# Optimization experiments

Hardware: AMD Instinct MI355X
Metric: run time of the kernel (lower is better)

Reference implementation:

```python
import jax, jax.numpy as jnp
import numpy as np

VOCAB, EMB, HID = 10, 32, 64
B, T = 256, 2048


def setup_inputs() -> dict:
    key = jax.random.key(0)
    ks = jax.random.split(key, 12)
    s = lambda k, shp, sc: jax.random.normal(k, shp, dtype=jnp.float32) * sc
    return {
        "num1": jax.random.randint(ks[0], (B, T), 0, VOCAB),
        "num2": jax.random.randint(ks[1], (B, T), 0, VOCAB),
        "E": s(ks[2], (VOCAB, EMB), 0.05),
        "Wx": s(ks[3], (EMB, 4 * HID), 1.0 / np.sqrt(EMB)),
        "Wh": s(ks[4], (HID, 4 * HID), 1.0 / np.sqrt(HID)),
        "b": jnp.zeros((4 * HID,), jnp.float32),
        "W1": s(ks[5], (2 * HID, 64), 1.0 / np.sqrt(2 * HID)),
        "b1": jnp.zeros((64,), jnp.float32),
        "W2": s(ks[6], (64, 32), 1.0 / np.sqrt(64)),
        "b2": jnp.zeros((32,), jnp.float32),
        "W3": s(ks[7], (32, VOCAB), 1.0 / np.sqrt(32)),
        "b3": jnp.zeros((VOCAB,), jnp.float32),
    }


def _lstm(x, Wx, Wh, b):
    # x: [B, T, EMB] -> hs: [B, T, HID]
    xz = jnp.einsum("btd,dg->btg", x, Wx) + b  # precompute input projection

    def step(carry, z_t):
        h, c = carry
        z = z_t + h @ Wh
        i, f, g, o = jnp.split(z, 4, axis=-1)  # Keras gate order: i, f, c, o
        i = jax.nn.sigmoid(i)
        f = jax.nn.sigmoid(f)
        g = jnp.tanh(g)
        o = jax.nn.sigmoid(o)
        c = f * c + i * g
        h = o * jnp.tanh(c)
        return (h, c), h

    bsz = x.shape[0]
    init = (jnp.zeros((bsz, HID), x.dtype), jnp.zeros((bsz, HID), x.dtype))
    _, hs = jax.lax.scan(step, init, jnp.swapaxes(xz, 0, 1))
    return jnp.swapaxes(hs, 0, 1)


def reference(num1, num2, E, Wx, Wh, b, W1, b1, W2, b2, W3, b3):
    x1 = E[num1]  # [B, T, EMB]
    x2 = E[num2]
    y1 = _lstm(x1, Wx, Wh, b)  # shared RNN layer (same weights)
    y2 = _lstm(x2, Wx, Wh, b)
    z = jnp.concatenate([y1, y2], axis=-1)  # [B, T, 128]
    w1 = jax.nn.relu(z @ W1 + b1)
    w2 = jax.nn.relu(w1 @ W2 + b2)
    return w2 @ W3 + b3  # [B, T, 10]
```

## Files before the change

kernel.cpp:

```cpp
#include <hip/hip_runtime.h>
#include <hip/hip_bf16.h>

#define BSZ    256
#define SEQT   2048
#define NVOCAB 10
#define DEMB   32
#define G4     256
#define BLK    384

typedef unsigned short u16;
typedef unsigned int   u32;
typedef float    v4f __attribute__((ext_vector_type(4)));
typedef u32      v4u __attribute__((ext_vector_type(4)));
typedef _Float16 v2h __attribute__((ext_vector_type(2)));

#define FLAG_OFF 0
#define XZ4_OFF  4
#define WHP_OFF  (XZ4_OFF + 2560)
#define W1P_OFF  (WHP_OFF + 8192)
#define W2P_OFF  (W1P_OFF + 4096)
#define W3_OFF   (W2P_OFF + 1024)
#define B1_OFF   (W3_OFF + 320)
#define B2_OFF   (B1_OFF + 64)
#define B3_OFF   (B2_OFF + 32)

__device__ __forceinline__ float bf2f(u16 x) {
    union { u32 u; float f; } v; v.u = ((u32)x) << 16; return v.f;
}
__device__ __forceinline__ u16 f2bf(float f) {
    union { float f; u32 u; } v; v.f = f;
    u32 r = v.u + 0x7fff + ((v.u >> 16) & 1);
    return (u16)(r >> 16);
}
__device__ __forceinline__ float ldw(const void* p, int i, bool isbf) {
    return isbf ? bf2f(((const u16*)p)[i]) : ((const float*)p)[i];
}
__device__ __forceinline__ float frcp(float x) { return __builtin_amdgcn_rcpf(x); }
__device__ __forceinline__ float sigf(float z) { return frcp(1.f + __expf(-z)); }
__device__ __forceinline__ u16 f2h(float x) {
    union { _Float16 h; u16 u; } v; v.h = (_Float16)x; return v.u;
}
__device__ __forceinline__ u32 packh2(float lo, float hi) {
    return (u32)f2h(lo) | ((u32)f2h(hi) << 16);
}
__device__ __forceinline__ float fdot2f(u32 a, u32 b, float c) {
    union { u32 u; v2h h; } ua, ub; ua.u = a; ub.u = b;
    return __builtin_amdgcn_fdot2(ua.h, ub.h, c, false);
}
__device__ __forceinline__ void dot4(float& acc, v4u w, v4u h) {
    acc = fdot2f(w.x, h.x, acc); acc = fdot2f(w.y, h.y, acc);
    acc = fdot2f(w.z, h.z, acc); acc = fdot2f(w.w, h.w, acc);
}

__global__ void init_kernel(const void* __restrict__ E,  const void* __restrict__ Wx,
                            const void* __restrict__ Wh, const void* __restrict__ bg,
                            const void* __restrict__ W1, const void* __restrict__ b1,
                            const void* __restrict__ W2, const void* __restrict__ b2,
                            const void* __restrict__ W3, const void* __restrict__ b3,
                            float* __restrict__ ws) {
    __shared__ int s_isbf;
    const int tid = threadIdx.x;
    if (tid == 0) s_isbf = 1;
    __syncthreads();
    {
        const u16* Eu = (const u16*)E;
        for (int i = tid; i < NVOCAB * DEMB; i += 256) {
            float v = bf2f(Eu[i]);
            if (!(fabsf(v) < 16.0f)) s_isbf = 0;
        }
    }
    __syncthreads();
    const bool isbf = (s_isbf != 0);
    if (tid == 0) ws[FLAG_OFF] = isbf ? 1.0f : 0.0f;
    u32* wsu = (u32*)ws;

    {
        const int g = tid >> 6, j = tid & 63, col = g * 64 + j;
        for (int v = 0; v < NVOCAB; v++) {
            float acc = ldw(bg, col, isbf);
            #pragma unroll
            for (int d = 0; d < DEMB; d++)
                acc += ldw(E, v * DEMB + d, isbf) * ldw(Wx, d * G4 + col, isbf);
            ws[XZ4_OFF + (v * 64 + j) * 4 + g] = acc;
        }
    }
    for (int i = tid; i < 8192; i += 256) {
        int l = i >> 7, rem = i & 127, g = rem >> 5, kk = rem & 31;
        int col = g * 64 + l;
        wsu[WHP_OFF + i] = packh2(ldw(Wh, (2 * kk) * G4 + col, isbf),
                                  ldw(Wh, (2 * kk + 1) * G4 + col, isbf));
    }
    for (int i = tid; i < 4096; i += 256) {
        int o = i >> 6, kk = i & 63;
        wsu[W1P_OFF + i] = packh2(ldw(W1, (2 * kk) * 64 + o, isbf),
                                  ldw(W1, (2 * kk + 1) * 64 + o, isbf));
    }
    for (int i = tid; i < 1024; i += 256) {
        int o = i >> 5, kk = i & 31;
        wsu[W2P_OFF + i] = packh2(ldw(W2, (2 * kk) * 32 + o, isbf),
                                  ldw(W2, (2 * kk + 1) * 32 + o, isbf));
    }
    for (int i = tid; i < 320; i += 256) ws[W3_OFF + i] = ldw(W3, i, isbf);
    if (tid < 64) ws[B1_OFF + tid] = ldw(b1, tid, isbf);
    if (tid < 32) ws[B2_OFF + tid] = ldw(b2, tid, isbf);
    if (tid < NVOCAB) ws[B3_OFF + tid] = ldw(b3, tid, isbf);
}

__global__ __launch_bounds__(BLK, 2) void lstm_fused(
    const int* __restrict__ num1, const int* __restrict__ num2,
    const float* __restrict__ ws, void* __restrict__ outv)
{
    __shared__ __align__(16) float xz4s[2560];
    __shared__ __align__(16) u16 hwinh[2][32][128];
    __shared__ __align__(16) u32 W1p[64 * 68];
    __shared__ __align__(16) u32 W2p[32 * 36];
    __shared__ float W3s[320];
    __shared__ __align__(16) u16 w1h[32 * 72];
    __shared__ __align__(16) float w2buf[32 * 36];
    __shared__ int idxs[2][2][32];

    const int tid = threadIdx.x, bb = blockIdx.x;
    const int wv = tid >> 6, l = tid & 63;
    const u32* wsu = (const u32*)ws;
    const bool outbf = (ws[FLAG_OFF] != 0.0f);

    for (int i = tid; i < 2560; i += BLK) xz4s[i] = ws[XZ4_OFF + i];
    for (int i = tid; i < 4096; i += BLK) { int o = i >> 6, kk = i & 63; W1p[o * 68 + kk] = wsu[W1P_OFF + i]; }
    for (int i = tid; i < 1024; i += BLK) { int o = i >> 5, kk = i & 31; W2p[o * 36 + kk] = wsu[W2P_OFF + i]; }
    for (int i = tid; i < 320; i += BLK) W3s[i] = ws[W3_OFF + i];
    if (tid < 128) hwinh[1][31][tid] = 0;
    if (tid < 64) { int c0 = tid >> 5, tt = tid & 31;
                    idxs[0][c0][tt] = (c0 == 0 ? num1 : num2)[bb * SEQT + tt]; }

    if (wv < 2) {
        v4u whq[32];
        {
            const v4u* whsrc = (const v4u*)(wsu + WHP_OFF) + (size_t)l * 32;
            #pragma unroll
            for (int i = 0; i < 32; i++) whq[i] = whsrc[i];
        }
        float c = 0.f;
        __syncthreads();
        for (int win = 0; win <= 64; win++) {
            #pragma unroll
            for (int i = 0; i < 32; i++) asm("" : "+v"(whq[i]));
            if (win < 64) {
                const int wb = win & 1;
                #pragma unroll 1
                for (int tt = 0; tt < 32; tt++) {
                    const int idx  = idxs[wb][wv][tt];
                    const int rbuf = (tt == 0) ? 1 - wb : wb;
                    const int rrow = (tt + 31) & 31;
                    const v4u* hp = (const v4u*)&hwinh[rbuf][rrow][wv * 64];
                    v4u hh[8];
                    #pragma unroll
                    for (int q = 0; q < 8; q++) hh[q] = hp[q];
                    v4f xzv = *(const v4f*)&xz4s[(idx * 64 + l) * 4];
                    float ai0 = 0.f, af0 = 0.f, ag0 = 0.f, ao0 = 0.f;
                    float ai1 = 0.f, af1 = 0.f, ag1 = 0.f, ao1 = 0.f;
                    #pragma unroll
                    for (int q = 0; q < 4; q++) {
                        dot4(ai0, whq[q],      hh[q]);
                        dot4(af0, whq[8 + q],  hh[q]);
                        dot4(ag0, whq[16 + q], hh[q]);
                        dot4(ao0, whq[24 + q], hh[q]);
                    }
                    #pragma unroll
                    for (int q = 4; q < 8; q++) {
                        dot4(ai1, whq[q],      hh[q]);
                        dot4(af1, whq[8 + q],  hh[q]);
                        dot4(ag1, whq[16 + q], hh[q]);
                        dot4(ao1, whq[24 + q], hh[q]);
                    }
                    float zi = ai0 + ai1 + xzv.x, zf = af0 + af1 + xzv.y;
                    float zg = ag0 + ag1 + xzv.z, zo = ao0 + ao1 + xzv.w;
                    float gi = sigf(zi), gf = sigf(zf);
                    float gG = 2.f * sigf(2.f * zg) - 1.f, go = sigf(zo);
                    c = gf * c + gi * gG;
                    float th = 1.f - 2.f * frcp(__expf(2.f * c) + 1.f);
                    hwinh[wb][tt][wv * 64 + l] = f2h(go * th);
                }
            }
            __syncthreads();
        }
    } else {
        const int mw = wv - 2;
        const int tb = mw * 8;
        const float b1o = ws[B1_OFF + l];
        const int th = l >> 5, o2 = l & 31;
        const float b2o = ws[B2_OFF + o2];
        const int tloc = l / 10, o3 = l - tloc * 10;
        const float b3o = (l < 40) ? ws[B3_OFF + o3] : 0.f;
        u16* outb = (u16*)outv; float* outf = (float*)outv;
        __syncthreads();
        float w3r[32];
        #pragma unroll
        for (int k = 0; k < 32; k++) w3r[k] = (l < 40) ? W3s[k * 10 + o3] : 0.f;
        for (int win = 0; win <= 64; win++) {
            if (win < 63 && mw < 2 && l < 32)
                idxs[(win + 1) & 1][mw][l] =
                    (mw == 0 ? num1 : num2)[bb * SEQT + (win + 1) * 32 + l];
            if (win >= 1) {
                const int pw = win - 1, pwb = pw & 1;
                float acc[8];
                #pragma unroll
                for (int i = 0; i < 8; i++) acc[i] = b1o;
                for (int kc = 0; kc < 16; kc++) {
                    v4u wq = *(const v4u*)&W1p[l * 68 + 4 * kc];
                    #pragma unroll
                    for (int i = 0; i < 8; i++) {
                        v4u hq = *(const v4u*)&hwinh[pwb][tb + i][8 * kc];
                        float a = acc[i];
                        a = fdot2f(wq.x, hq.x, a); a = fdot2f(wq.y, hq.y, a);
                        a = fdot2f(wq.z, hq.z, a); a = fdot2f(wq.w, hq.w, a);
                        acc[i] = a;
                    }
                }
                #pragma unroll
                for (int i = 0; i < 8; i++)
                    w1h[(tb + i) * 72 + l] = f2h(fmaxf(acc[i], 0.f));
                float a2[4];
                #pragma unroll
                for (int i = 0; i < 4; i++) a2[i] = b2o;
                for (int kc = 0; kc < 8; kc++) {
                    v4u wq = *(const v4u*)&W2p[o2 * 36 + 4 * kc];
                    #pragma unroll
                    for (int i = 0; i < 4; i++) {
                        v4u hq = *(const v4u*)&w1h[(tb + th * 4 + i) * 72 + 8 * kc];
                        float a = a2[i];
                        a = fdot2f(wq.x, hq.x, a); a = fdot2f(wq.y, hq.y, a);
                        a = fdot2f(wq.z, hq.z, a); a = fdot2f(wq.w, hq.w, a);
                        a2[i] = a;
                    }
                }
                #pragma unroll
                for (int i = 0; i < 4; i++)
                    w2buf[(tb + th * 4 + i) * 36 + o2] = fmaxf(a2[i], 0.f);
                if (l < 40) {
                    #pragma unroll
                    for (int i = 0; i < 2; i++) {
                        const int tk = tb + tloc * 2 + i;
                        const v4f* wp = (const v4f*)&w2buf[tk * 36];
                        float a = b3o;
                        #pragma unroll
                        for (int q = 0; q < 8; q++) {
                            v4f w4 = wp[q];
                            a += w3r[4 * q]     * w4.x + w3r[4 * q + 1] * w4.y
                               + w3r[4 * q + 2] * w4.z + w3r[4 * q + 3] * w4.w;
                        }
                        const size_t oi = (size_t)(bb * SEQT + pw * 32 + tk) * NVOCAB + o3;
                        if (outbf) outb[oi] = f2bf(a); else outf[oi] = a;
                    }
                }
            }
            __syncthreads();
        }
    }
}

extern "C" void kernel_launch(void* const* d_in, const int* in_sizes, int n_in,
                              void* d_out, int out_size, void* d_ws, size_t ws_size,
                              hipStream_t stream) {
    const int* num1 = (const int*)d_in[0];
    const int* num2 = (const int*)d_in[1];
    float* ws = (float*)d_ws;

    hipLaunchKernelGGL(init_kernel, dim3(1), dim3(256), 0, stream,
                       d_in[2], d_in[3], d_in[4], d_in[5], d_in[6], d_in[7],
                       d_in[8], d_in[9], d_in[10], d_in[11], ws);
    hipLaunchKernelGGL(lstm_fused, dim3(BSZ), dim3(BLK), 0, stream,
                       num1, num2, ws, d_out);
}
```

Measured before the change: 981.5 us.

## Split LSTM gates across four waves per chain and serialize MLP after recurrence

Each LSTM chain is now spread over four wavefronts, one per gate, instead of one wavefront computing all four gates. Each gate wave holds only its slice of Wh in registers and exchanges activations through shared memory with a block-wide barrier every timestep. The MLP head no longer runs in dedicated waves concurrently with the recurrence. All 8 waves now run it after each 32-step window. The change shortens the per-step dependent dot-product chain but adds a __syncthreads per timestep and removes the overlap between recurrence and MLP.

```diff
diff --git a/kernel.cpp b/kernel.cpp
--- a/kernel.cpp
+++ b/kernel.cpp
@@ -6,7 +6,7 @@
 #define NVOCAB 10
 #define DEMB   32
 #define G4     256
-#define BLK    384
+#define BLK    512
 
 typedef unsigned short u16;
 typedef unsigned int   u32;
@@ -106,155 +106,140 @@
     if (tid < NVOCAB) ws[B3_OFF + tid] = ldw(b3, tid, isbf);
 }
 
-__global__ __launch_bounds__(BLK, 2) void lstm_fused(
+__global__ __launch_bounds__(BLK) void lstm_fused(
     const int* __restrict__ num1, const int* __restrict__ num2,
     const float* __restrict__ ws, void* __restrict__ outv)
 {
-    __shared__ __align__(16) float xz4s[2560];
+    __shared__ __align__(16) float xzg[4 * 10 * 64];
     __shared__ __align__(16) u16 hwinh[2][32][128];
+    __shared__ __align__(16) u16 hpriv[8][64];
+    __shared__ __align__(16) float acts[2][2][4][64];
     __shared__ __align__(16) u32 W1p[64 * 68];
     __shared__ __align__(16) u32 W2p[32 * 36];
     __shared__ float W3s[320];
+    __shared__ float B1s[64], B2s[32], B3s[16];
     __shared__ __align__(16) u16 w1h[32 * 72];
     __shared__ __align__(16) float w2buf[32 * 36];
     __shared__ int idxs[2][2][32];
 
     const int tid = threadIdx.x, bb = blockIdx.x;
     const int wv = tid >> 6, l = tid & 63;
+    const int ch = wv >> 2, g = wv & 3;
     const u32* wsu = (const u32*)ws;
     const bool outbf = (ws[FLAG_OFF] != 0.0f);
 
-    for (int i = tid; i < 2560; i += BLK) xz4s[i] = ws[XZ4_OFF + i];
+    for (int t = tid; t < 2560; t += BLK) {
+        int gg = t / 640, rem = t - gg * 640;
+        xzg[t] = ws[XZ4_OFF + rem * 4 + gg];
+    }
     for (int i = tid; i < 4096; i += BLK) { int o = i >> 6, kk = i & 63; W1p[o * 68 + kk] = wsu[W1P_OFF + i]; }
     for (int i = tid; i < 1024; i += BLK) { int o = i >> 5, kk = i & 31; W2p[o * 36 + kk] = wsu[W2P_OFF + i]; }
     for (int i = tid; i < 320; i += BLK) W3s[i] = ws[W3_OFF + i];
-    if (tid < 128) hwinh[1][31][tid] = 0;
+    if (tid < 64) B1s[tid] = ws[B1_OFF + tid];
+    if (tid < 32) B2s[tid] = ws[B2_OFF + tid];
+    if (tid < NVOCAB) B3s[tid] = ws[B3_OFF + tid];
+    hpriv[wv][l] = 0;
     if (tid < 64) { int c0 = tid >> 5, tt = tid & 31;
                     idxs[0][c0][tt] = (c0 == 0 ? num1 : num2)[bb * SEQT + tt]; }
 
-    if (wv < 2) {
-        v4u whq[32];
-        {
-            const v4u* whsrc = (const v4u*)(wsu + WHP_OFF) + (size_t)l * 32;
-            #pragma unroll
-            for (int i = 0; i < 32; i++) whq[i] = whsrc[i];
-        }
-        float c = 0.f;
+    const v4u* whsrc = (const v4u*)(wsu + WHP_OFF) + ((size_t)l * 32 + g * 8);
+    v4u wqA0 = whsrc[0], wqA1 = whsrc[1], wqA2 = whsrc[2], wqA3 = whsrc[3];
+    v4u wqB0 = whsrc[4], wqB1 = whsrc[5], wqB2 = whsrc[6], wqB3 = whsrc[7];
+    float c = 0.f;
+
+    const int tb = wv * 4;
+    const int th = l >> 5, o2 = l & 31;
+    const int tloc = l / 10, o3 = l - tloc * 10;
+    u16* outb = (u16*)outv; float* outf = (float*)outv;
+
+    __syncthreads();
+
+    for (int win = 0; win <= 64; win++) {
+        #define PINQ(x) asm("" : "+v"(x))
+        PINQ(wqA0); PINQ(wqA1); PINQ(wqA2); PINQ(wqA3);
+        PINQ(wqB0); PINQ(wqB1); PINQ(wqB2); PINQ(wqB3);
+        #undef PINQ
+        if (win < 64) {
+            const int wb = win & 1;
+            if (win < 63 && g == 3 && l < 32)
+                idxs[(win + 1) & 1][ch][l] =
+                    (ch == 0 ? num1 : num2)[bb * SEQT + (win + 1) * 32 + l];
+            #pragma unroll 1
+            for (int tt = 0; tt < 32; tt++) {
+                const int p = tt & 1;
+                const int idx = idxs[wb][ch][tt];
+                const v4u* hp = (const v4u*)&hpriv[wv][0];
+                float za = 0.f, zb = 0.f;
+                {
+                    v4u h0 = hp[0], h1 = hp[1], h2 = hp[2], h3 = hp[3];
+                    dot4(za, wqA0, h0); dot4(za, wqA1, h1);
+                    dot4(za, wqA2, h2); dot4(za, wqA3, h3);
+                }
+                {
+                    v4u h4 = hp[4], h5 = hp[5], h6 = hp[6], h7 = hp[7];
+                    dot4(zb, wqB0, h4); dot4(zb, wqB1, h5);
+                    dot4(zb, wqB2, h6); dot4(zb, wqB3, h7);
+                }
+                float z = za + zb + xzg[g * 640 + idx * 64 + l];
+                float act = (g == 2) ? (2.f * sigf(2.f * z) - 1.f)
+                                     : sigf(z);
+                acts[p][ch][g][l] = act;
+                __syncthreads();
+                float ai = acts[p][ch][0][l], af = acts[p][ch][1][l];
+                float ag = acts[p][ch][2][l], ao = acts[p][ch][3][l];
+                c = af * c + ai * ag;
+                float thh = 1.f - 2.f * frcp(__expf(2.f * c) + 1.f);
+                u16 hb = f2h(ao * thh);
+                hpriv[wv][l] = hb;
+                if (g == 0) hwinh[wb][tt][ch * 64 + l] = hb;
+            }
+        }
         __syncthreads();
-        for (int win = 0; win <= 64; win++) {
-            #pragma unroll
-            for (int i = 0; i < 32; i++) asm("" : "+v"(whq[i]));
-            if (win < 64) {
-                const int wb = win & 1;
-                #pragma unroll 1
-                for (int tt = 0; tt < 32; tt++) {
-                    const int idx  = idxs[wb][wv][tt];
-                    const int rbuf = (tt == 0) ? 1 - wb : wb;
-                    const int rrow = (tt + 31) & 31;
-                    const v4u* hp = (const v4u*)&hwinh[rbuf][rrow][wv * 64];
-                    v4u hh[8];
-                    #pragma unroll
-                    for (int q = 0; q < 8; q++) hh[q] = hp[q];
-                    v4f xzv = *(const v4f*)&xz4s[(idx * 64 + l) * 4];
-                    float ai0 = 0.f, af0 = 0.f, ag0 = 0.f, ao0 = 0.f;
-                    float ai1 = 0.f, af1 = 0.f, ag1 = 0.f, ao1 = 0.f;
-                    #pragma unroll
-                    for (int q = 0; q < 4; q++) {
-                        dot4(ai0, whq[q],      hh[q]);
-                        dot4(af0, whq[8 + q],  hh[q]);
-                        dot4(ag0, whq[16 + q], hh[q]);
-                        dot4(ao0, whq[24 + q], hh[q]);
-                    }
-                    #pragma unroll
-                    for (int q = 4; q < 8; q++) {
-                        dot4(ai1, whq[q],      hh[q]);
-                        dot4(af1, whq[8 + q],  hh[q]);
-                        dot4(ag1, whq[16 + q], hh[q]);
-                        dot4(ao1, whq[24 + q], hh[q]);
-                    }
-                    float zi = ai0 + ai1 + xzv.x, zf = af0 + af1 + xzv.y;
-                    float zg = ag0 + ag1 + xzv.z, zo = ao0 + ao1 + xzv.w;
-                    float gi = sigf(zi), gf = sigf(zf);
-                    float gG = 2.f * sigf(2.f * zg) - 1.f, go = sigf(zo);
-                    c = gf * c + gi * gG;
-                    float th = 1.f - 2.f * frcp(__expf(2.f * c) + 1.f);
-                    hwinh[wb][tt][wv * 64 + l] = f2h(go * th);
+        if (win >= 1) {
+            const int pw = win - 1, pwb = pw & 1;
+            const float b1o = B1s[l];
+            float acc0 = b1o, acc1 = b1o, acc2 = b1o, acc3 = b1o;
+            for (int kc = 0; kc < 16; kc++) {
+                v4u wq = *(const v4u*)&W1p[l * 68 + 4 * kc];
+                v4u q0 = *(const v4u*)&hwinh[pwb][tb + 0][8 * kc];
+                v4u q1 = *(const v4u*)&hwinh[pwb][tb + 1][8 * kc];
+                v4u q2 = *(const v4u*)&hwinh[pwb][tb + 2][8 * kc];
+                v4u q3 = *(const v4u*)&hwinh[pwb][tb + 3][8 * kc];
+                dot4(acc0, wq, q0); dot4(acc1, wq, q1);
+                dot4(acc2, wq, q2); dot4(acc3, wq, q3);
+            }
+            w1h[(tb + 0) * 72 + l] = f2h(fmaxf(acc0, 0.f));
+            w1h[(tb + 1) * 72 + l] = f2h(fmaxf(acc1, 0.f));
+            w1h[(tb + 2) * 72 + l] = f2h(fmaxf(acc2, 0.f));
+            w1h[(tb + 3) * 72 + l] = f2h(fmaxf(acc3, 0.f));
+            const float b2o = B2s[o2];
+            float a20 = b2o, a21 = b2o;
+            for (int kc = 0; kc < 8; kc++) {
+                v4u wq = *(const v4u*)&W2p[o2 * 36 + 4 * kc];
+                v4u q0 = *(const v4u*)&w1h[(tb + th * 2 + 0) * 72 + 8 * kc];
+                v4u q1 = *(const v4u*)&w1h[(tb + th * 2 + 1) * 72 + 8 * kc];
+                dot4(a20, wq, q0); dot4(a21, wq, q1);
+            }
+            w2buf[(tb + th * 2 + 0) * 36 + o2] = fmaxf(a20, 0.f);
+            w2buf[(tb + th * 2 + 1) * 36 + o2] = fmaxf(a21, 0.f);
+            if (l < 40) {
+                float w3r[32];
+                #pragma unroll
+                for (int k = 0; k < 32; k++) w3r[k] = W3s[k * 10 + o3];
+                const int tk = tb + tloc;
+                const v4f* wp = (const v4f*)&w2buf[tk * 36];
+                float a = B3s[o3];
+                #pragma unroll
+                for (int q = 0; q < 8; q++) {
+                    v4f w4 = wp[q];
+                    a += w3r[4 * q]     * w4.x + w3r[4 * q + 1] * w4.y
+                       + w3r[4 * q + 2] * w4.z + w3r[4 * q + 3] * w4.w;
                 }
-            }
-            __syncthreads();
-        }
-    } else {
-        const int mw = wv - 2;
-        const int tb = mw * 8;
-        const float b1o = ws[B1_OFF + l];
-        const int th = l >> 5, o2 = l & 31;
-        const float b2o = ws[B2_OFF + o2];
-        const int tloc = l / 10, o3 = l - tloc * 10;
-        const float b3o = (l < 40) ? ws[B3_OFF + o3] : 0.f;
-        u16* outb = (u16*)outv; float* outf = (float*)outv;
+                const size_t oi = (size_t)(bb * SEQT + pw * 32 + tk) * NVOCAB + o3;
+                if (outbf) outb[oi] = f2bf(a); else outf[oi] = a;
+            }
+        }
         __syncthreads();
-        float w3r[32];
-        #pragma unroll
-        for (int k = 0; k < 32; k++) w3r[k] = (l < 40) ? W3s[k * 10 + o3] : 0.f;
-        for (int win = 0; win <= 64; win++) {
-            if (win < 63 && mw < 2 && l < 32)
-                idxs[(win + 1) & 1][mw][l] =
-                    (mw == 0 ? num1 : num2)[bb * SEQT + (win + 1) * 32 + l];
-            if (win >= 1) {
-                const int pw = win - 1, pwb = pw & 1;
-                float acc[8];
-                #pragma unroll
-                for (int i = 0; i < 8; i++) acc[i] = b1o;
-                for (int kc = 0; kc < 16; kc++) {
-                    v4u wq = *(const v4u*)&W1p[l * 68 + 4 * kc];
-                    #pragma unroll
-                    for (int i = 0; i < 8; i++) {
-                        v4u hq = *(const v4u*)&hwinh[pwb][tb + i][8 * kc];
-                        float a = acc[i];
-                        a = fdot2f(wq.x, hq.x, a); a = fdot2f(wq.y, hq.y, a);
-                        a = fdot2f(wq.z, hq.z, a); a = fdot2f(wq.w, hq.w, a);
-                        acc[i] = a;
-                    }
-                }
-                #pragma unroll
-                for (int i = 0; i < 8; i++)
-                    w1h[(tb + i) * 72 + l] = f2h(fmaxf(acc[i], 0.f));
-                float a2[4];
-                #pragma unroll
-                for (int i = 0; i < 4; i++) a2[i] = b2o;
-                for (int kc = 0; kc < 8; kc++) {
-                    v4u wq = *(const v4u*)&W2p[o2 * 36 + 4 * kc];
-                    #pragma unroll
-                    for (int i = 0; i < 4; i++) {
-                        v4u hq = *(const v4u*)&w1h[(tb + th * 4 + i) * 72 + 8 * kc];
-                        float a = a2[i];
-                        a = fdot2f(wq.x, hq.x, a); a = fdot2f(wq.y, hq.y, a);
-                        a = fdot2f(wq.z, hq.z, a); a = fdot2f(wq.w, hq.w, a);
-                        a2[i] = a;
-                    }
-                }
-                #pragma unroll
-                for (int i = 0; i < 4; i++)
-                    w2buf[(tb + th * 4 + i) * 36 + o2] = fmaxf(a2[i], 0.f);
-                if (l < 40) {
-                    #pragma unroll
-                    for (int i = 0; i < 2; i++) {
-                        const int tk = tb + tloc * 2 + i;
-                        const v4f* wp = (const v4f*)&w2buf[tk * 36];
-                        float a = b3o;
-                        #pragma unroll
-                        for (int q = 0; q < 8; q++) {
-                            v4f w4 = wp[q];
-                            a += w3r[4 * q]     * w4.x + w3r[4 * q + 1] * w4.y
-                               + w3r[4 * q + 2] * w4.z + w3r[4 * q + 3] * w4.w;
-                        }
-                        const size_t oi = (size_t)(bb * SEQT + pw * 32 + tk) * NVOCAB + o3;
-                        if (outbf) outb[oi] = f2bf(a); else outf[oi] = a;
-                    }
-                }
-            }
-            __syncthreads();
-        }
     }
 }
 
```

Measured after the change: 1.219 ms. 24.2% more time.

## Run both LSTM chains in one wavefront to interleave independent recurrences

Applied to the files above, without the earlier changes.

The two recurrent LSTM chains (num1 and num2) now run in a single wavefront instead of two, each thread holding two cell states and interleaving both dot-product chains so their independent latencies overlap. The block shrinks from 384 to 320 threads and the occupancy hint in launch_bounds is dropped. This aims to hide the serial per-step latency through instruction-level parallelism within one wave. It doubles per-thread work and register pressure, and the MLP wave indices shift by one.

```diff
diff --git a/kernel.cpp b/kernel.cpp
--- a/kernel.cpp
+++ b/kernel.cpp
@@ -6,7 +6,7 @@
 #define NVOCAB 10
 #define DEMB   32
 #define G4     256
-#define BLK    384
+#define BLK    320
 
 typedef unsigned short u16;
 typedef unsigned int   u32;
@@ -106,7 +106,7 @@
     if (tid < NVOCAB) ws[B3_OFF + tid] = ldw(b3, tid, isbf);
 }
 
-__global__ __launch_bounds__(BLK, 2) void lstm_fused(
+__global__ __launch_bounds__(BLK) void lstm_fused(
     const int* __restrict__ num1, const int* __restrict__ num2,
     const float* __restrict__ ws, void* __restrict__ outv)
 {
@@ -132,14 +132,14 @@
     if (tid < 64) { int c0 = tid >> 5, tt = tid & 31;
                     idxs[0][c0][tt] = (c0 == 0 ? num1 : num2)[bb * SEQT + tt]; }
 
-    if (wv < 2) {
+    if (wv == 0) {
         v4u whq[32];
         {
             const v4u* whsrc = (const v4u*)(wsu + WHP_OFF) + (size_t)l * 32;
             #pragma unroll
             for (int i = 0; i < 32; i++) whq[i] = whsrc[i];
         }
-        float c = 0.f;
+        float c0 = 0.f, c1 = 0.f;
         __syncthreads();
         for (int win = 0; win <= 64; win++) {
             #pragma unroll
@@ -148,43 +148,54 @@
                 const int wb = win & 1;
                 #pragma unroll 1
                 for (int tt = 0; tt < 32; tt++) {
-                    const int idx  = idxs[wb][wv][tt];
+                    const int idx0 = idxs[wb][0][tt];
+                    const int idx1 = idxs[wb][1][tt];
                     const int rbuf = (tt == 0) ? 1 - wb : wb;
                     const int rrow = (tt + 31) & 31;
-                    const v4u* hp = (const v4u*)&hwinh[rbuf][rrow][wv * 64];
-                    v4u hh[8];
-                    #pragma unroll
-                    for (int q = 0; q < 8; q++) hh[q] = hp[q];
-                    v4f xzv = *(const v4f*)&xz4s[(idx * 64 + l) * 4];
-                    float ai0 = 0.f, af0 = 0.f, ag0 = 0.f, ao0 = 0.f;
-                    float ai1 = 0.f, af1 = 0.f, ag1 = 0.f, ao1 = 0.f;
+                    const v4u* hp0 = (const v4u*)&hwinh[rbuf][rrow][0];
+                    const v4u* hp1 = (const v4u*)&hwinh[rbuf][rrow][64];
+                    v4f xzv0 = *(const v4f*)&xz4s[(idx0 * 64 + l) * 4];
+                    v4f xzv1 = *(const v4f*)&xz4s[(idx1 * 64 + l) * 4];
+                    float i0a = 0.f, f0a = 0.f, g0a = 0.f, o0a = 0.f;
+                    float i0b = 0.f, f0b = 0.f, g0b = 0.f, o0b = 0.f;
+                    float i1a = 0.f, f1a = 0.f, g1a = 0.f, o1a = 0.f;
+                    float i1b = 0.f, f1b = 0.f, g1b = 0.f, o1b = 0.f;
                     #pragma unroll
                     for (int q = 0; q < 4; q++) {
-                        dot4(ai0, whq[q],      hh[q]);
-                        dot4(af0, whq[8 + q],  hh[q]);
-                        dot4(ag0, whq[16 + q], hh[q]);
-                        dot4(ao0, whq[24 + q], hh[q]);
+                        v4u h0 = hp0[q], h1 = hp1[q];
+                        dot4(i0a, whq[q],      h0); dot4(i1a, whq[q],      h1);
+                        dot4(f0a, whq[8 + q],  h0); dot4(f1a, whq[8 + q],  h1);
+                        dot4(g0a, whq[16 + q], h0); dot4(g1a, whq[16 + q], h1);
+                        dot4(o0a, whq[24 + q], h0); dot4(o1a, whq[24 + q], h1);
                     }
                     #pragma unroll
                     for (int q = 4; q < 8; q++) {
-                        dot4(ai1, whq[q],      hh[q]);
-                        dot4(af1, whq[8 + q],  hh[q]);
-                        dot4(ag1, whq[16 + q], hh[q]);
-                        dot4(ao1, whq[24 + q], hh[q]);
-                    }
-                    float zi = ai0 + ai1 + xzv.x, zf = af0 + af1 + xzv.y;
-                    float zg = ag0 + ag1 + xzv.z, zo = ao0 + ao1 + xzv.w;
-                    float gi = sigf(zi), gf = sigf(zf);
-                    float gG = 2.f * sigf(2.f * zg) - 1.f, go = sigf(zo);
-                    c = gf * c + gi * gG;
-                    float th = 1.f - 2.f * frcp(__expf(2.f * c) + 1.f);
-                    hwinh[wb][tt][wv * 64 + l] = f2h(go * th);
+                        v4u h0 = hp0[q], h1 = hp1[q];
+                        dot4(i0b, whq[q],      h0); dot4(i1b, whq[q],      h1);
+                        dot4(f0b, whq[8 + q],  h0); dot4(f1b, whq[8 + q],  h1);
+                        dot4(g0b, whq[16 + q], h0); dot4(g1b, whq[16 + q], h1);
+                        dot4(o0b, whq[24 + q], h0); dot4(o1b, whq[24 + q], h1);
+                    }
+                    float zi0 = i0a + i0b + xzv0.x, zf0 = f0a + f0b + xzv0.y;
+                    float zg0 = g0a + g0b + xzv0.z, zo0 = o0a + o0b + xzv0.w;
+                    float zi1 = i1a + i1b + xzv1.x, zf1 = f1a + f1b + xzv1.y;
+                    float zg1 = g1a + g1b + xzv1.z, zo1 = o1a + o1b + xzv1.w;
+                    float gi0 = sigf(zi0), gf0 = sigf(zf0);
+                    float gi1 = sigf(zi1), gf1 = sigf(zf1);
+                    float gG0 = 2.f * sigf(2.f * zg0) - 1.f, go0 = sigf(zo0);
+                    float gG1 = 2.f * sigf(2.f * zg1) - 1.f, go1 = sigf(zo1);
+                    c0 = gf0 * c0 + gi0 * gG0;
+                    c1 = gf1 * c1 + gi1 * gG1;
+                    float th0 = 1.f - 2.f * frcp(__expf(2.f * c0) + 1.f);
+                    float th1 = 1.f - 2.f * frcp(__expf(2.f * c1) + 1.f);
+                    hwinh[wb][tt][l]      = f2h(go0 * th0);
+                    hwinh[wb][tt][64 + l] = f2h(go1 * th1);
                 }
             }
             __syncthreads();
         }
     } else {
-        const int mw = wv - 2;
+        const int mw = wv - 1;
         const int tb = mw * 8;
         const float b1o = ws[B1_OFF + l];
         const int th = l >> 5, o2 = l & 31;
```

New measurement: 2.361 ms. 141% more time.

## Compute LSTM recurrent matvec with MFMA 16x16x32 f16 instead of fdot2

Applied to the files above, without the earlier changes.

Replaces the per-lane fdot2 recurrent h·Wh product with 32 MFMA 16x16x32 f16 instructions per step, using a broadcast h vector as the A operand and a new fragment layout for Wh packed in init. Each lane then selects its gate values from the MFMA outputs. The aim is to shorten the serial per-timestep latency on the recurrence critical path. In exchange, most of the matrix-core work is wasted because only one row of the A operand is useful, and MFMA latency plus the selection logic could cost more than the fdot2 chain did.

```diff
diff --git a/kernel.cpp b/kernel.cpp
--- a/kernel.cpp
+++ b/kernel.cpp
@@ -13,6 +13,7 @@
 typedef float    v4f __attribute__((ext_vector_type(4)));
 typedef u32      v4u __attribute__((ext_vector_type(4)));
 typedef _Float16 v2h __attribute__((ext_vector_type(2)));
+typedef _Float16 v8h __attribute__((ext_vector_type(8)));
 
 #define FLAG_OFF 0
 #define XZ4_OFF  4
@@ -46,10 +47,6 @@
 __device__ __forceinline__ float fdot2f(u32 a, u32 b, float c) {
     union { u32 u; v2h h; } ua, ub; ua.u = a; ub.u = b;
     return __builtin_amdgcn_fdot2(ua.h, ub.h, c, false);
-}
-__device__ __forceinline__ void dot4(float& acc, v4u w, v4u h) {
-    acc = fdot2f(w.x, h.x, acc); acc = fdot2f(w.y, h.y, acc);
-    acc = fdot2f(w.z, h.z, acc); acc = fdot2f(w.w, h.w, acc);
 }
 
 __global__ void init_kernel(const void* __restrict__ E,  const void* __restrict__ Wx,
@@ -85,10 +82,12 @@
         }
     }
     for (int i = tid; i < 8192; i += 256) {
-        int l = i >> 7, rem = i & 127, g = rem >> 5, kk = rem & 31;
-        int col = g * 64 + l;
-        wsu[WHP_OFF + i] = packh2(ldw(Wh, (2 * kk) * G4 + col, isbf),
-                                  ldw(Wh, (2 * kk + 1) * G4 + col, isbf));
+        int f = i >> 8, rem = i & 255, lane = rem >> 2, q = rem & 3;
+        int t = f >> 1, kk = f & 1;
+        int c  = t * 16 + (lane & 15);
+        int k0 = kk * 32 + (lane >> 4) * 8 + 2 * q;
+        wsu[WHP_OFF + i] = packh2(ldw(Wh, k0 * G4 + c, isbf),
+                                  ldw(Wh, (k0 + 1) * G4 + c, isbf));
     }
     for (int i = tid; i < 4096; i += 256) {
         int o = i >> 6, kk = i & 63;
@@ -133,52 +132,48 @@
                     idxs[0][c0][tt] = (c0 == 0 ? num1 : num2)[bb * SEQT + tt]; }
 
     if (wv < 2) {
-        v4u whq[32];
+        const int ch = wv;
+        union u2h { v4u u; v8h h; };
+        v8h bq[32];
         {
-            const v4u* whsrc = (const v4u*)(wsu + WHP_OFF) + (size_t)l * 32;
+            const v4u* bsrc = (const v4u*)(wsu + WHP_OFF);
             #pragma unroll
-            for (int i = 0; i < 32; i++) whq[i] = whsrc[i];
+            for (int f = 0; f < 32; f++) { u2h cv; cv.u = bsrc[f * 64 + l]; bq[f] = cv.h; }
         }
         float c = 0.f;
         __syncthreads();
         for (int win = 0; win <= 64; win++) {
-            #pragma unroll
-            for (int i = 0; i < 32; i++) asm("" : "+v"(whq[i]));
             if (win < 64) {
                 const int wb = win & 1;
                 #pragma unroll 1
                 for (int tt = 0; tt < 32; tt++) {
-                    const int idx  = idxs[wb][wv][tt];
+                    const int idx  = idxs[wb][ch][tt];
                     const int rbuf = (tt == 0) ? 1 - wb : wb;
                     const int rrow = (tt + 31) & 31;
-                    const v4u* hp = (const v4u*)&hwinh[rbuf][rrow][wv * 64];
-                    v4u hh[8];
-                    #pragma unroll
-                    for (int q = 0; q < 8; q++) hh[q] = hp[q];
+                    const v4u* hpA = (const v4u*)&hwinh[rbuf][rrow][ch * 64];
+                    u2h a0c, a1c;
+                    a0c.u = hpA[l >> 4];
+                    a1c.u = hpA[4 + (l >> 4)];
                     v4f xzv = *(const v4f*)&xz4s[(idx * 64 + l) * 4];
-                    float ai0 = 0.f, af0 = 0.f, ag0 = 0.f, ao0 = 0.f;
-                    float ai1 = 0.f, af1 = 0.f, ag1 = 0.f, ao1 = 0.f;
-                    #pragma unroll
-                    for (int q = 0; q < 4; q++) {
-                        dot4(ai0, whq[q],      hh[q]);
-                        dot4(af0, whq[8 + q],  hh[q]);
-                        dot4(ag0, whq[16 + q], hh[q]);
-                        dot4(ao0, whq[24 + q], hh[q]);
-                    }
-                    #pragma unroll
-                    for (int q = 4; q < 8; q++) {
-                        dot4(ai1, whq[q],      hh[q]);
-                        dot4(af1, whq[8 + q],  hh[q]);
-                        dot4(ag1, whq[16 + q], hh[q]);
-                        dot4(ao1, whq[24 + q], hh[q]);
-                    }
-                    float zi = ai0 + ai1 + xzv.x, zf = af0 + af1 + xzv.y;
-                    float zg = ag0 + ag1 + xzv.z, zo = ao0 + ao1 + xzv.w;
+                    v4f acc[16];
+                    #pragma unroll
+                    for (int t = 0; t < 16; t++) {
+                        v4f z4 = {0.f, 0.f, 0.f, 0.f};
+                        z4 = __builtin_amdgcn_mfma_f32_16x16x32_f16(a0c.h, bq[2 * t],     z4, 0, 0, 0);
+                        z4 = __builtin_amdgcn_mfma_f32_16x16x32_f16(a1c.h, bq[2 * t + 1], z4, 0, 0, 0);
+                        acc[t] = z4;
+                    }
+                    const int grp = l >> 4;
+                    float zi = (grp == 0) ? acc[0].x  : (grp == 1) ? acc[1].x  : (grp == 2) ? acc[2].x  : acc[3].x;
+                    float zf = (grp == 0) ? acc[4].x  : (grp == 1) ? acc[5].x  : (grp == 2) ? acc[6].x  : acc[7].x;
+                    float zg = (grp == 0) ? acc[8].x  : (grp == 1) ? acc[9].x  : (grp == 2) ? acc[10].x : acc[11].x;
+                    float zo = (grp == 0) ? acc[12].x : (grp == 1) ? acc[13].x : (grp == 2) ? acc[14].x : acc[15].x;
+                    zi += xzv.x; zf += xzv.y; zg += xzv.z; zo += xzv.w;
                     float gi = sigf(zi), gf = sigf(zf);
                     float gG = 2.f * sigf(2.f * zg) - 1.f, go = sigf(zo);
                     c = gf * c + gi * gG;
                     float th = 1.f - 2.f * frcp(__expf(2.f * c) + 1.f);
-                    hwinh[wb][tt][wv * 64 + l] = f2h(go * th);
+                    hwinh[wb][tt][ch * 64 + l] = f2h(go * th);
                 }
             }
             __syncthreads();
```

Measured after the change: 1.128 ms. 14.9% more time.
